# Kernel tuning notes

Measured on AMD Instinct MI355X. Metric: run time of the kernel, lower is better.

The kernel has to match this reference:

```python
import jax, jax.numpy as jnp
import numpy as np

N, G, E, H, M = 200000, 16, 400000, 400000, 800000
DN, DG, DE, DH, DM = 128, 32, 128, 64, 64
K_EDGE, K_HYP, AK = 32, 3, 8  # fixed incident edges per node, nodes per hyperedge, attention key size / heads
LN_EPS = 1e-3  # keras LayerNormalization default epsilon


def setup_inputs() -> dict:
    key = jax.random.key(0)
    ks = jax.random.split(key, 20)
    p = lambda k, shp: (0.02 * jax.random.normal(k, shp, dtype=jnp.float32))
    return {
        "nodes": jax.random.normal(ks[0], (N, DN), dtype=jnp.float32),
        "globals_": jax.random.normal(ks[1], (G, DG), dtype=jnp.float32),
        "n_node": jnp.full((G,), N // G, dtype=jnp.int32),
        "edges": jax.random.normal(ks[2], (E, DE), dtype=jnp.float32),
        "edge_ind": jax.random.randint(ks[3], (N, K_EDGE), 0, E, dtype=jnp.int32),
        "hfeat": jax.random.normal(ks[4], (H, DH), dtype=jnp.float32),
        "hind": jax.random.randint(ks[5], (H, K_HYP), 0, N, dtype=jnp.int32),
        "mfeat": jax.random.normal(ks[6], (M, DM), dtype=jnp.float32),
        "mind": jax.random.randint(ks[7], (M,), 0, N, dtype=jnp.int32),
        "Wq": p(ks[8], (DN, AK)), "bq": jnp.zeros((AK,), jnp.float32),
        "Wk": p(ks[9], (DE, AK)), "bk": jnp.zeros((AK,), jnp.float32),
        "Wc": p(ks[10], (4, AK, AK)), "bc": jnp.zeros((AK,), jnp.float32),
        "W1": p(ks[11], (DN + DG + AK + DH + DM, 256)), "b1": jnp.zeros((256,), jnp.float32),
        "W2": p(ks[12], (256, 128)), "b2": jnp.zeros((128,), jnp.float32),
        "ln_g": jnp.ones((128,), jnp.float32), "ln_b": jnp.zeros((128,), jnp.float32),
    }


def reference(nodes, globals_, n_node, edges, edge_ind, hfeat, hind, mfeat, mind,
              Wq, bq, Wk, bk, Wc, bc, W1, b1, W2, b2, ln_g, ln_b):
    n = nodes.shape[0]
    # _one_to_segments: repeat globals per node (graph id from n_node offsets)
    gid = jnp.searchsorted(jnp.cumsum(n_node), jnp.arange(n), side="right")
    g_per_node = globals_[gid]  # [N, DG]

    # EDGES branch: fixed-number multi-head attention over incident edges
    q = nodes @ Wq + bq   # [N, AK]
    k = edges @ Wk + bk   # [E, AK]
    # Conv1D(kernel=4, 'same') on a length-1 sequence: only kernel tap 1 touches data
    q_mh = q @ Wc[1] + bc  # [N, heads]
    k_mh = k @ Wc[1] + bc  # [E, heads]
    ek = k_mh[edge_ind]                         # [N, K, heads] gathered keys (= values)
    attn = jax.nn.softmax(q_mh[:, None, :] * ek, axis=1)
    edge_agg = jnp.sum(attn * ek, axis=1)       # [N, heads] (flatten of [N,1,heads])

    # _one_to_fixed_number: scatter hyperedge features to their K_HYP member nodes
    hh, kk, dh = hfeat.shape[0], hind.shape[1], hfeat.shape[1]
    h_agg = jax.ops.segment_sum(
        jnp.broadcast_to(hfeat[:, None, :], (hh, kk, dh)).reshape(hh * kk, dh),
        hind.reshape(-1), num_segments=n)       # [N, DH]

    # _one_to_unsorted_segments
    m_agg = jax.ops.segment_sum(mfeat, mind, num_segments=n)  # [N, DM]

    x = jnp.concatenate([nodes, g_per_node, edge_agg, h_agg, m_agg], axis=1)
    h1 = jax.nn.relu(x @ W1 + b1)
    h2 = jax.nn.relu(h1 @ W2 + b2)
    mu = jnp.mean(h2, axis=-1, keepdims=True)
    var = jnp.var(h2, axis=-1, keepdims=True)
    out = (h2 - mu) * jax.lax.rsqrt(var + LN_EPS) * ln_g + ln_b
    return out
```

## Files before the change

### kernel.cpp

```cpp
#include <hip/hip_runtime.h>
#include <hip/hip_bf16.h>
#include <math.h>

#define N_NODES 200000
#define N_E     400000
#define N_H     400000
#define N_M     800000
#define HK3     1200000
#define DIM_N   128
#define K_EDGE  32
#define D1      296
#define KX      320
#define LN_EPS  1e-3f
#define TILE    32
#define CHUNK   1024
#define NCH     196
#define NB_E    12500
#define NB_N    6250
#define NB_C    7813

typedef __attribute__((ext_vector_type(8))) short bf16x8;
typedef __attribute__((ext_vector_type(4))) float f32x4;
typedef unsigned short ushort_t;

#define SWZ(rr) (((rr) & 7) << 4)

__device__ __forceinline__ short f2bf(float f) {
    unsigned u = __float_as_uint(f);
    unsigned r = (u + 0x7fffu + ((u >> 16) & 1u)) >> 16;
    return (short)r;
}
__device__ __forceinline__ float bf2f(ushort_t u) {
    return __uint_as_float(((unsigned)u) << 16);
}
__device__ __forceinline__ void split2(float v, short& hi, short& lo) {
    hi = f2bf(v);
    float r = v - __uint_as_float(((unsigned)(ushort_t)hi) << 16);
    lo = f2bf(r);
}

__global__ void prep_weights(const float* __restrict__ Wq, const float* __restrict__ bq,
                             const float* __restrict__ Wk, const float* __restrict__ bk,
                             const float* __restrict__ Wc, const float* __restrict__ bc,
                             float* Wqc, float* bqc, float* Wkc, float* bkc) {
    int t = blockIdx.x * 256 + threadIdx.x;
    const float* Wc1 = Wc + 64;
    if (t < 128 * 8) {
        int i = t >> 3, o = t & 7;
        float s = 0.f, s2 = 0.f;
        for (int a = 0; a < 8; ++a) {
            float w = Wc1[a * 8 + o];
            s  += Wq[i * 8 + a] * w;
            s2 += Wk[i * 8 + a] * w;
        }
        Wqc[t] = s;
        Wkc[t] = s2;
    } else if (t < 128 * 8 + 8) {
        int o = t - 1024;
        float s = 0.f, s2 = 0.f;
        for (int a = 0; a < 8; ++a) {
            float w = Wc1[a * 8 + o];
            s  += bq[a] * w;
            s2 += bk[a] * w;
        }
        bqc[o] = s + bc[o];
        bkc[o] = s2 + bc[o];
    }
}

__global__ void prep_wF(const float* __restrict__ W1, const float* __restrict__ W2,
                        short* __restrict__ W1Fh, short* __restrict__ W1Fl,
                        short* __restrict__ W2Fh, short* __restrict__ W2Fl) {
    int g = blockIdx.x * 256 + threadIdx.x;
    if (g < 10240) {
        int l = g & 63, f = g >> 6;
        int s = f % 10, nt = (f / 10) & 3, wid = f / 40;
        int col = wid * 64 + nt * 16 + (l & 15);
        int k0 = s * 32 + (l >> 4) * 8;
        #pragma unroll
        for (int j = 0; j < 8; ++j) {
            int k = k0 + j;
            float w = (k < D1) ? W1[k * 256 + col] : 0.f;
            short hi, lo; split2(w, hi, lo);
            W1Fh[g * 8 + j] = hi; W1Fl[g * 8 + j] = lo;
        }
    } else if (g < 14336) {
        int u = g - 10240;
        int l = u & 63, f = u >> 6;
        int s = f & 7, nt = (f >> 3) & 1, wid = f >> 4;
        int col = wid * 32 + nt * 16 + (l & 15);
        int k0 = s * 32 + (l >> 4) * 8;
        #pragma unroll
        for (int j = 0; j < 8; ++j) {
            float w = W2[(k0 + j) * 128 + col];
            short hi, lo; split2(w, hi, lo);
            W2Fh[u * 8 + j] = hi; W2Fl[u * 8 + j] = lo;
        }
    }
}

__device__ __forceinline__ void mh_body(const float* __restrict__ feat,
                                        const float* __restrict__ Wf,
                                        const float* __restrict__ bf_,
                                        ushort_t* __restrict__ out8,
                                        int blk, int tid,
                                        float* el, float* wlT, float* bl) {
    for (int i = tid; i < 1024; i += 256) {
        int h = i >> 7, k = i & 127;
        wlT[h * 132 + k] = Wf[k * 8 + h];
    }
    if (tid < 8) bl[tid] = bf_[tid];
    long e0 = (long)blk * 32;
    const float4* ep = (const float4*)feat + e0 * 32;
    for (int it = 0; it < 4; ++it) {
        int idx = it * 256 + tid;
        int e = idx >> 5, f = idx & 31;
        float4 v = ep[e * 32 + f];
        float* d = &el[e * 132 + f * 4];
        d[0] = v.x; d[1] = v.y; d[2] = v.z; d[3] = v.w;
    }
    __syncthreads();
    int e = tid >> 3, h = tid & 7;
    float acc = bl[h];
    const float* er = &el[e * 132];
    const float* wr = &wlT[h * 132];
    #pragma unroll 8
    for (int i = 0; i < 128; i += 4) {
        float4 ev = *(const float4*)&er[i];
        float4 wv = *(const float4*)&wr[i];
        acc += ev.x * wv.x + ev.y * wv.y + ev.z * wv.z + ev.w * wv.w;
    }
    out8[(e0 + e) * 8 + h] = (ushort_t)f2bf(acc);
}

__global__ __launch_bounds__(256) void aux1_kernel(
    const float* __restrict__ edges, const float* __restrict__ Wkc,
    const float* __restrict__ bkc, ushort_t* __restrict__ kmh,
    const float* __restrict__ nodes, const float* __restrict__ Wqc,
    const float* __restrict__ bqc, ushort_t* __restrict__ qmh,
    const int* __restrict__ hind, const int* __restrict__ mind,
    int* __restrict__ cnth, int* __restrict__ cntm)
{
    __shared__ __align__(16) float el[32 * 132];
    __shared__ __align__(16) float wlT[8 * 132];
    __shared__ float bl[8];
    int b = blockIdx.x, tid = threadIdx.x;
    if (b < NB_E) {
        mh_body(edges, Wkc, bkc, kmh, b, tid, el, wlT, bl);
    } else if (b < NB_E + NB_N) {
        mh_body(nodes, Wqc, bqc, qmh, b - NB_E, tid, el, wlT, bl);
    } else {
        int t = (b - NB_E - NB_N) * 256 + tid;
        if (t < HK3)              atomicAdd(&cnth[hind[t]], 1);
        else if (t < HK3 + N_M)   atomicAdd(&cntm[mind[t - HK3]], 1);
    }
}

__global__ void zero_ints(int* __restrict__ p, int n) {
    int stride = gridDim.x * blockDim.x;
    for (int i = blockIdx.x * blockDim.x + threadIdx.x; i < n; i += stride) p[i] = 0;
}

__global__ __launch_bounds__(256) void sum_chunks(const int* __restrict__ cnth,
                                                  const int* __restrict__ cntm,
                                                  int* __restrict__ bsum) {
    int b = blockIdx.x;
    const int* cnt = (b < NCH) ? cnth : cntm;
    int base = ((b < NCH) ? b : b - NCH) * CHUNK;
    int tid = threadIdx.x;
    int s = 0;
    #pragma unroll
    for (int i = 0; i < 4; ++i) {
        int idx = base + i * 256 + tid;
        if (idx < N_NODES) s += cnt[idx];
    }
    __shared__ int sb[4];
    for (int d = 1; d < 64; d <<= 1) s += __shfl_xor(s, d);
    if ((tid & 63) == 0) sb[tid >> 6] = s;
    __syncthreads();
    if (tid == 0) bsum[b] = sb[0] + sb[1] + sb[2] + sb[3];
}

__global__ __launch_bounds__(256) void scan_sums(int* __restrict__ bsum) {
    __shared__ int sh[2][256];
    int tid = threadIdx.x;
    sh[0][tid] = (tid < NCH) ? bsum[tid] : 0;
    sh[1][tid] = (tid < NCH) ? bsum[NCH + tid] : 0;
    __syncthreads();
    for (int d = 1; d < 256; d <<= 1) {
        int v0 = (tid >= d) ? sh[0][tid - d] : 0;
        int v1 = (tid >= d) ? sh[1][tid - d] : 0;
        __syncthreads();
        sh[0][tid] += v0; sh[1][tid] += v1;
        __syncthreads();
    }
    if (tid < NCH) {
        bsum[tid]       = tid ? sh[0][tid - 1] : 0;
        bsum[NCH + tid] = tid ? sh[1][tid - 1] : 0;
    }
}

__global__ __launch_bounds__(256) void scan_chunks(const int* __restrict__ cnth,
                                                   const int* __restrict__ cntm,
                                                   const int* __restrict__ bsum,
                                                   int* __restrict__ offh, int* __restrict__ woffh,
                                                   int* __restrict__ offm, int* __restrict__ woffm) {
    int b = blockIdx.x;
    bool ish = (b < NCH);
    const int* cnt = ish ? cnth : cntm;
    int c = ish ? b : b - NCH;
    int* off  = ish ? offh  : offm;
    int* woff = ish ? woffh : woffm;
    int base = c * CHUNK;
    int tid = threadIdx.x;
    __shared__ int lds[CHUNK];
    __shared__ int tsum[256];
    #pragma unroll
    for (int i = 0; i < 4; ++i) {
        int idx = base + i * 256 + tid;
        lds[i * 256 + tid] = (idx < N_NODES) ? cnt[idx] : 0;
    }
    __syncthreads();
    int v0 = lds[tid * 4], v1 = lds[tid * 4 + 1], v2 = lds[tid * 4 + 2], v3 = lds[tid * 4 + 3];
    int tot = v0 + v1 + v2 + v3;
    tsum[tid] = tot;
    __syncthreads();
    for (int d = 1; d < 256; d <<= 1) {
        int v = (tid >= d) ? tsum[tid - d] : 0;
        __syncthreads();
        tsum[tid] += v;
        __syncthreads();
    }
    int pre = tsum[tid] - tot + bsum[b];
    int4 o;
    o.x = pre; o.y = pre + v0; o.z = pre + v0 + v1; o.w = pre + v0 + v1 + v2;
    int idx = base + tid * 4;
    if (idx + 3 < N_NODES) {
        *(int4*)(off + idx)  = o;
        *(int4*)(woff + idx) = o;
    } else {
        if (idx     < N_NODES) { off[idx]     = o.x; woff[idx]     = o.x; }
        if (idx + 1 < N_NODES) { off[idx + 1] = o.y; woff[idx + 1] = o.y; }
        if (idx + 2 < N_NODES) { off[idx + 2] = o.z; woff[idx + 2] = o.z; }
        if (idx + 3 < N_NODES) { off[idx + 3] = o.w; woff[idx + 3] = o.w; }
    }
}

__global__ void fill_kernel(const int* __restrict__ hind, const int* __restrict__ mind,
                            int* __restrict__ woffh, int* __restrict__ woffm,
                            int* __restrict__ listh, int* __restrict__ listm) {
    int t = blockIdx.x * 256 + threadIdx.x;
    if (t < HK3) {
        int node = hind[t];
        int pos = atomicAdd(&woffh[node], 1);
        listh[pos] = t / 3;
    } else if (t < HK3 + N_M) {
        int m = t - HK3;
        int node = mind[m];
        int pos = atomicAdd(&woffm[node], 1);
        listm[pos] = m;
    }
}

__global__ __launch_bounds__(256) void main_kernel(
    const float* __restrict__ nodes, const float* __restrict__ globals_,
    const int* __restrict__ n_node, const int* __restrict__ edge_ind,
    const ushort_t* __restrict__ kmh, const ushort_t* __restrict__ qmh,
    const float* __restrict__ hfeat, const int* __restrict__ offh,
    const int* __restrict__ woffh, const int* __restrict__ listh,
    const float* __restrict__ mfeat, const int* __restrict__ offm,
    const int* __restrict__ woffm, const int* __restrict__ listm,
    const short* __restrict__ W1Fh, const short* __restrict__ W1Fl, const float* __restrict__ b1,
    const short* __restrict__ W2Fh, const short* __restrict__ W2Fl, const float* __restrict__ b2,
    const float* __restrict__ ln_g, const float* __restrict__ ln_b,
    float* __restrict__ out)
{
    __shared__ __align__(16) char buf[20480];
    __shared__ int eind[32 * 33];
    __shared__ float mrs[64];

    int tid = threadIdx.x;
    int n0 = blockIdx.x * TILE;
    char* xhi = buf;

    const float4* np4 = (const float4*)nodes;
    #pragma unroll
    for (int it = 0; it < 4; ++it) {
        int idx = it * 256 + tid;
        int r = idx >> 5, c4 = idx & 31;
        float4 v = np4[(size_t)(n0 + r) * 32 + c4];
        short4 hi;
        hi.x = f2bf(v.x); hi.y = f2bf(v.y); hi.z = f2bf(v.z); hi.w = f2bf(v.w);
        *(short4*)(xhi + r * 640 + ((c4 * 8) ^ SWZ(r))) = hi;
    }
    {
        int nn0 = n_node[0];
        int r = tid >> 3, c4 = tid & 7;
        int gid = (n0 + r) / nn0;
        float4 v = ((const float4*)globals_)[gid * 8 + c4];
        short4 hi;
        hi.x = f2bf(v.x); hi.y = f2bf(v.y); hi.z = f2bf(v.z); hi.w = f2bf(v.w);
        *(short4*)(xhi + r * 640 + ((256 + c4 * 8) ^ SWZ(r))) = hi;
    }
    {
        int r = tid >> 3, q = tid & 7;
        int n = n0 + r;
        float a[8];
        #pragma unroll
        for (int i = 0; i < 8; ++i) a[i] = 0.f;
        int e0 = offh[n], e1 = woffh[n];
        int e = e0;
        #define ACC8(U, V) do { \
            a[0] += (U).x; a[1] += (U).y; a[2] += (U).z; a[3] += (U).w; \
            a[4] += (V).x; a[5] += (V).y; a[6] += (V).z; a[7] += (V).w; } while (0)
        for (; e + 4 <= e1; e += 4) {
            int i0 = listh[e], i1 = listh[e + 1], i2 = listh[e + 2], i3 = listh[e + 3];
            const float4* p0 = (const float4*)(hfeat + (size_t)i0 * 64 + q * 8);
            const float4* p1 = (const float4*)(hfeat + (size_t)i1 * 64 + q * 8);
            const float4* p2 = (const float4*)(hfeat + (size_t)i2 * 64 + q * 8);
            const float4* p3 = (const float4*)(hfeat + (size_t)i3 * 64 + q * 8);
            float4 u0 = p0[0], v0 = p0[1];
            float4 u1 = p1[0], v1 = p1[1];
            float4 u2 = p2[0], v2 = p2[1];
            float4 u3 = p3[0], v3 = p3[1];
            ACC8(u0, v0); ACC8(u1, v1); ACC8(u2, v2); ACC8(u3, v3);
        }
        for (; e < e1; ++e) {
            const float4* p = (const float4*)(hfeat + (size_t)listh[e] * 64 + q * 8);
            float4 u = p[0], v = p[1];
            ACC8(u, v);
        }
        {
            bf16x8 hi;
            #pragma unroll
            for (int i = 0; i < 8; ++i) hi[i] = f2bf(a[i]);
            *(bf16x8*)(xhi + r * 640 + ((336 + q * 16) ^ SWZ(r))) = hi;
        }
        #pragma unroll
        for (int i = 0; i < 8; ++i) a[i] = 0.f;
        e0 = offm[n]; e1 = woffm[n];
        e = e0;
        for (; e + 4 <= e1; e += 4) {
            int i0 = listm[e], i1 = listm[e + 1], i2 = listm[e + 2], i3 = listm[e + 3];
            const float4* p0 = (const float4*)(mfeat + (size_t)i0 * 64 + q * 8);
            const float4* p1 = (const float4*)(mfeat + (size_t)i1 * 64 + q * 8);
            const float4* p2 = (const float4*)(mfeat + (size_t)i2 * 64 + q * 8);
            const float4* p3 = (const float4*)(mfeat + (size_t)i3 * 64 + q * 8);
            float4 u0 = p0[0], v0 = p0[1];
            float4 u1 = p1[0], v1 = p1[1];
            float4 u2 = p2[0], v2 = p2[1];
            float4 u3 = p3[0], v3 = p3[1];
            ACC8(u0, v0); ACC8(u1, v1); ACC8(u2, v2); ACC8(u3, v3);
        }
        for (; e < e1; ++e) {
            const float4* p = (const float4*)(mfeat + (size_t)listm[e] * 64 + q * 8);
            float4 u = p[0], v = p[1];
            ACC8(u, v);
        }
        #undef ACC8
        {
            bf16x8 hi;
            #pragma unroll
            for (int i = 0; i < 8; ++i) hi[i] = f2bf(a[i]);
            *(bf16x8*)(xhi + r * 640 + ((464 + q * 16) ^ SWZ(r))) = hi;
        }
    }
    if (tid < 192) {
        short4 z = { 0, 0, 0, 0 };
        int r = tid / 6, j = tid % 6;
        *(short4*)(xhi + r * 640 + ((592 + j * 8) ^ SWZ(r))) = z;
    }
    #pragma unroll
    for (int it = 0; it < 4; ++it) {
        int idx = it * 256 + tid;
        int r = idx >> 5, j = idx & 31;
        eind[r * 33 + j] = edge_ind[(size_t)(n0 + r) * 32 + j];
    }
    __syncthreads();

    {
        int r = tid & 31, h = tid >> 5;
        float qv = bf2f(qmh[(size_t)(n0 + r) * 8 + h]);
        float m = -INFINITY, s = 0.f, wv = 0.f;
        for (int j = 0; j < K_EDGE; ++j) {
            int e = eind[r * 33 + j];
            float v = bf2f(kmh[(size_t)e * 8 + h]);
            float l = qv * v;
            float mn = fmaxf(m, l);
            float fac = __expf(m - mn);
            float p = __expf(l - mn);
            s = s * fac + p;
            wv = wv * fac + p * v;
            m = mn;
        }
        *(short*)(xhi + r * 640 + ((320 + h * 2) ^ SWZ(r))) = f2bf(wv / s);
    }
    __syncthreads();

    int wid = tid >> 6, lane = tid & 63;
    int arow = lane & 15, kgrp = lane >> 4;
    f32x4 c1[2][4];
    #pragma unroll
    for (int mt = 0; mt < 2; ++mt)
        #pragma unroll
        for (int nt = 0; nt < 4; ++nt)
            c1[mt][nt] = (f32x4){0.f, 0.f, 0.f, 0.f};
    const bf16x8* w1h = (const bf16x8*)W1Fh;
    const bf16x8* w1l = (const bf16x8*)W1Fl;
    for (int s = 0; s < 10; ++s) {
        int kb = (s * 32 + kgrp * 8) * 2;
        bf16x8 ahv[2], bh[4], bl[4];
        #pragma unroll
        for (int mt = 0; mt < 2; ++mt) {
            int rr = mt * 16 + arow;
            ahv[mt] = *(const bf16x8*)(xhi + rr * 640 + (kb ^ SWZ(rr)));
        }
        #pragma unroll
        for (int nt = 0; nt < 4; ++nt) {
            size_t fi = ((size_t)(wid * 4 + nt) * 10 + s) * 64 + lane;
            bh[nt] = w1h[fi];
            bl[nt] = w1l[fi];
        }
        #pragma unroll
        for (int mt = 0; mt < 2; ++mt)
            #pragma unroll
            for (int nt = 0; nt < 4; ++nt) {
                c1[mt][nt] = __builtin_amdgcn_mfma_f32_16x16x32_bf16(ahv[mt], bh[nt], c1[mt][nt], 0, 0, 0);
                c1[mt][nt] = __builtin_amdgcn_mfma_f32_16x16x32_bf16(ahv[mt], bl[nt], c1[mt][nt], 0, 0, 0);
            }
    }
    __syncthreads();
    char* h1p = buf;
    #pragma unroll
    for (int nt = 0; nt < 4; ++nt) {
        int col = wid * 64 + nt * 16 + arow;
        float bb = b1[col];
        #pragma unroll
        for (int mt = 0; mt < 2; ++mt)
            #pragma unroll
            for (int i = 0; i < 4; ++i) {
                int rr = mt * 16 + kgrp * 4 + i;
                float v = fmaxf(c1[mt][nt][i] + bb, 0.f);
                *(short*)(h1p + rr * 512 + ((col * 2) ^ SWZ(rr))) = f2bf(v);
            }
    }
    __syncthreads();

    f32x4 c2[2][2];
    #pragma unroll
    for (int mt = 0; mt < 2; ++mt)
        #pragma unroll
        for (int nt = 0; nt < 2; ++nt)
            c2[mt][nt] = (f32x4){0.f, 0.f, 0.f, 0.f};
    const bf16x8* w2h = (const bf16x8*)W2Fh;
    const bf16x8* w2l = (const bf16x8*)W2Fl;
    for (int s = 0; s < 8; ++s) {
        int kb = (s * 32 + kgrp * 8) * 2;
        bf16x8 ahv[2], bh[2], bl[2];
        #pragma unroll
        for (int mt = 0; mt < 2; ++mt) {
            int rr = mt * 16 + arow;
            ahv[mt] = *(const bf16x8*)(h1p + rr * 512 + (kb ^ SWZ(rr)));
        }
        #pragma unroll
        for (int nt = 0; nt < 2; ++nt) {
            size_t fi = ((size_t)(wid * 2 + nt) * 8 + s) * 64 + lane;
            bh[nt] = w2h[fi];
            bl[nt] = w2l[fi];
        }
        #pragma unroll
        for (int mt = 0; mt < 2; ++mt)
            #pragma unroll
            for (int nt = 0; nt < 2; ++nt) {
                c2[mt][nt] = __builtin_amdgcn_mfma_f32_16x16x32_bf16(ahv[mt], bh[nt], c2[mt][nt], 0, 0, 0);
                c2[mt][nt] = __builtin_amdgcn_mfma_f32_16x16x32_bf16(ahv[mt], bl[nt], c2[mt][nt], 0, 0, 0);
            }
    }
    __syncthreads();
    #pragma unroll
    for (int nt = 0; nt < 2; ++nt) {
        int col = wid * 32 + nt * 16 + arow;
        float bb = b2[col];
        #pragma unroll
        for (int mt = 0; mt < 2; ++mt)
            #pragma unroll
            for (int i = 0; i < 4; ++i) {
                int rr = mt * 16 + kgrp * 4 + i;
                *(float*)(buf + rr * 528 + col * 4) = fmaxf(c2[mt][nt][i] + bb, 0.f);
            }
    }
    __syncthreads();

    {
        int r = tid >> 3, q = tid & 7;
        const float* row = (const float*)(buf + r * 528) + q * 16;
        float s = 0.f, sq = 0.f;
        #pragma unroll
        for (int j = 0; j < 4; ++j) {
            float4 v = *(const float4*)(row + j * 4);
            s  += v.x + v.y + v.z + v.w;
            sq += v.x * v.x + v.y * v.y + v.z * v.z + v.w * v.w;
        }
        s  += __shfl_xor(s, 1);  sq += __shfl_xor(sq, 1);
        s  += __shfl_xor(s, 2);  sq += __shfl_xor(sq, 2);
        s  += __shfl_xor(s, 4);  sq += __shfl_xor(sq, 4);
        if (q == 0) {
            float mean = s * (1.f / 128.f);
            float var = sq * (1.f / 128.f) - mean * mean;
            mrs[r] = mean;
            mrs[32 + r] = rsqrtf(var + LN_EPS);
        }
    }
    __syncthreads();
    #pragma unroll
    for (int it = 0; it < 4; ++it) {
        int idx = it * 256 + tid;
        int r = idx >> 5, c4 = idx & 31;
        float4 v = *(const float4*)(buf + r * 528 + c4 * 16);
        float mu = mrs[r], rs = mrs[32 + r];
        float4 g = ((const float4*)ln_g)[c4];
        float4 bb = ((const float4*)ln_b)[c4];
        float4 o;
        o.x = (v.x - mu) * rs * g.x + bb.x;
        o.y = (v.y - mu) * rs * g.y + bb.y;
        o.z = (v.z - mu) * rs * g.z + bb.z;
        o.w = (v.w - mu) * rs * g.w + bb.w;
        ((float4*)out)[(size_t)(n0 + r) * 32 + c4] = o;
    }
}

extern "C" void kernel_launch(void* const* d_in, const int* in_sizes, int n_in,
                              void* d_out, int out_size, void* d_ws, size_t ws_size,
                              hipStream_t stream) {
    const float* nodes    = (const float*)d_in[0];
    const float* globals_ = (const float*)d_in[1];
    const int*   n_node   = (const int*)  d_in[2];
    const float* edges    = (const float*)d_in[3];
    const int*   edge_ind = (const int*)  d_in[4];
    const float* hfeat    = (const float*)d_in[5];
    const int*   hind     = (const int*)  d_in[6];
    const float* mfeat    = (const float*)d_in[7];
    const int*   mind     = (const int*)  d_in[8];
    const float* Wq       = (const float*)d_in[9];
    const float* bq       = (const float*)d_in[10];
    const float* Wk       = (const float*)d_in[11];
    const float* bk       = (const float*)d_in[12];
    const float* Wc       = (const float*)d_in[13];
    const float* bc       = (const float*)d_in[14];
    const float* W1       = (const float*)d_in[15];
    const float* b1       = (const float*)d_in[16];
    const float* W2       = (const float*)d_in[17];
    const float* b2       = (const float*)d_in[18];
    const float* ln_g     = (const float*)d_in[19];
    const float* ln_b     = (const float*)d_in[20];
    float* out = (float*)d_out;

    char* w = (char*)d_ws;
    size_t off = 0;
    auto take = [&](size_t bytes) -> char* {
        char* p = w + off;
        off = (off + bytes + 255) & ~(size_t)255;
        return p;
    };
    float*    Wqc  = (float*)take(1024 * 4);
    float*    bqc  = (float*)take(8 * 4);
    float*    Wkc  = (float*)take(1024 * 4);
    float*    bkc  = (float*)take(8 * 4);
    short*    W1Fh = (short*)take(256 * KX * 2);
    short*    W1Fl = (short*)take(256 * KX * 2);
    short*    W2Fh = (short*)take(128 * 256 * 2);
    short*    W2Fl = (short*)take(128 * 256 * 2);
    ushort_t* kmh  = (ushort_t*)take((size_t)N_E * 8 * 2);
    ushort_t* qmh  = (ushort_t*)take((size_t)N_NODES * 8 * 2);
    int*      cnth = (int*)take((size_t)N_NODES * 4);
    int*      cntm = (int*)take((size_t)N_NODES * 4);
    int*      offh = (int*)take((size_t)N_NODES * 4);
    int*      woffh= (int*)take((size_t)N_NODES * 4);
    int*      offm = (int*)take((size_t)N_NODES * 4);
    int*      woffm= (int*)take((size_t)N_NODES * 4);
    int*      listh= (int*)take((size_t)HK3 * 4);
    int*      listm= (int*)take((size_t)N_M * 4);
    int*      bsum = (int*)take(2 * NCH * 4);
    (void)ws_size;

    prep_weights<<<5, 256, 0, stream>>>(Wq, bq, Wk, bk, Wc, bc, Wqc, bqc, Wkc, bkc);
    prep_wF<<<56, 256, 0, stream>>>(W1, W2, W1Fh, W1Fl, W2Fh, W2Fl);
    zero_ints<<<512, 256, 0, stream>>>(cnth, 2 * N_NODES);
    aux1_kernel<<<NB_E + NB_N + NB_C, 256, 0, stream>>>(
        edges, Wkc, bkc, kmh, nodes, Wqc, bqc, qmh, hind, mind, cnth, cntm);
    sum_chunks<<<2 * NCH, 256, 0, stream>>>(cnth, cntm, bsum);
    scan_sums<<<1, 256, 0, stream>>>(bsum);
    scan_chunks<<<2 * NCH, 256, 0, stream>>>(cnth, cntm, bsum, offh, woffh, offm, woffm);
    fill_kernel<<<(HK3 + N_M + 255) / 256, 256, 0, stream>>>(hind, mind, woffh, woffm, listh, listm);
    main_kernel<<<N_NODES / TILE, 256, 0, stream>>>(
        nodes, globals_, n_node, edge_ind, kmh, qmh,
        hfeat, offh, woffh, listh, mfeat, offm, woffm, listm,
        W1Fh, W1Fl, b1, W2Fh, W2Fl, b2, ln_g, ln_b, out);
}
```

Measured before the change: 691.1 us.

## Vectorize CSR fill, interleave hyper/message gathers, raise MFMA wave priority

The fill kernel now handles four indices per thread using int4 loads, cutting the thread count by four while keeping the atomics. In the main kernel, the hyperedge and message gather loops are interleaved so both streams issue loads together, which exposes more memory-level parallelism. s_setprio is raised around the MFMA loops to favour matrix-issuing waves. The interleaving adds register pressure that could reduce occupancy.

```diff
diff --git a/kernel.cpp b/kernel.cpp
--- a/kernel.cpp
+++ b/kernel.cpp
@@ -246,19 +246,26 @@
     }
 }
 
-__global__ void fill_kernel(const int* __restrict__ hind, const int* __restrict__ mind,
-                            int* __restrict__ woffh, int* __restrict__ woffm,
-                            int* __restrict__ listh, int* __restrict__ listm) {
+__global__ __launch_bounds__(256) void fill_kernel(
+    const int* __restrict__ hind, const int* __restrict__ mind,
+    int* __restrict__ woffh, int* __restrict__ woffm,
+    int* __restrict__ listh, int* __restrict__ listm) {
     int t = blockIdx.x * 256 + threadIdx.x;
-    if (t < HK3) {
-        int node = hind[t];
-        int pos = atomicAdd(&woffh[node], 1);
-        listh[pos] = t / 3;
-    } else if (t < HK3 + N_M) {
-        int m = t - HK3;
-        int node = mind[m];
-        int pos = atomicAdd(&woffm[node], 1);
-        listm[pos] = m;
+    if (t < HK3 / 4) {
+        int4 nd = ((const int4*)hind)[t];
+        int base = t * 4;
+        int p0 = atomicAdd(&woffh[nd.x], 1); listh[p0] = (base    ) / 3;
+        int p1 = atomicAdd(&woffh[nd.y], 1); listh[p1] = (base + 1) / 3;
+        int p2 = atomicAdd(&woffh[nd.z], 1); listh[p2] = (base + 2) / 3;
+        int p3 = atomicAdd(&woffh[nd.w], 1); listh[p3] = (base + 3) / 3;
+    } else if (t < HK3 / 4 + N_M / 4) {
+        int u = t - HK3 / 4;
+        int4 nd = ((const int4*)mind)[u];
+        int base = u * 4;
+        int p0 = atomicAdd(&woffm[nd.x], 1); listm[p0] = base;
+        int p1 = atomicAdd(&woffm[nd.y], 1); listm[p1] = base + 1;
+        int p2 = atomicAdd(&woffm[nd.z], 1); listm[p2] = base + 2;
+        int p3 = atomicAdd(&woffm[nd.w], 1); listm[p3] = base + 3;
     }
 }
 
@@ -305,63 +312,70 @@
     {
         int r = tid >> 3, q = tid & 7;
         int n = n0 + r;
-        float a[8];
-        #pragma unroll
-        for (int i = 0; i < 8; ++i) a[i] = 0.f;
-        int e0 = offh[n], e1 = woffh[n];
-        int e = e0;
-        #define ACC8(U, V) do { \
-            a[0] += (U).x; a[1] += (U).y; a[2] += (U).z; a[3] += (U).w; \
-            a[4] += (V).x; a[5] += (V).y; a[6] += (V).z; a[7] += (V).w; } while (0)
-        for (; e + 4 <= e1; e += 4) {
-            int i0 = listh[e], i1 = listh[e + 1], i2 = listh[e + 2], i3 = listh[e + 3];
-            const float4* p0 = (const float4*)(hfeat + (size_t)i0 * 64 + q * 8);
-            const float4* p1 = (const float4*)(hfeat + (size_t)i1 * 64 + q * 8);
-            const float4* p2 = (const float4*)(hfeat + (size_t)i2 * 64 + q * 8);
-            const float4* p3 = (const float4*)(hfeat + (size_t)i3 * 64 + q * 8);
-            float4 u0 = p0[0], v0 = p0[1];
-            float4 u1 = p1[0], v1 = p1[1];
-            float4 u2 = p2[0], v2 = p2[1];
-            float4 u3 = p3[0], v3 = p3[1];
-            ACC8(u0, v0); ACC8(u1, v1); ACC8(u2, v2); ACC8(u3, v3);
-        }
-        for (; e < e1; ++e) {
-            const float4* p = (const float4*)(hfeat + (size_t)listh[e] * 64 + q * 8);
+        float ah[8], am[8];
+        #pragma unroll
+        for (int i = 0; i < 8; ++i) { ah[i] = 0.f; am[i] = 0.f; }
+        int eh = offh[n], ehe = woffh[n];
+        int em = offm[n], eme = woffm[n];
+        #define ACC8(A, U, V) do { \
+            A[0] += (U).x; A[1] += (U).y; A[2] += (U).z; A[3] += (U).w; \
+            A[4] += (V).x; A[5] += (V).y; A[6] += (V).z; A[7] += (V).w; } while (0)
+        for (; eh + 4 <= ehe && em + 4 <= eme; eh += 4, em += 4) {
+            int h0 = listh[eh], h1_ = listh[eh + 1], h2_ = listh[eh + 2], h3 = listh[eh + 3];
+            int m0 = listm[em], m1 = listm[em + 1], m2 = listm[em + 2], m3 = listm[em + 3];
+            const float4* ph0 = (const float4*)(hfeat + (size_t)h0  * 64 + q * 8);
+            const float4* ph1 = (const float4*)(hfeat + (size_t)h1_ * 64 + q * 8);
+            const float4* ph2 = (const float4*)(hfeat + (size_t)h2_ * 64 + q * 8);
+            const float4* ph3 = (const float4*)(hfeat + (size_t)h3  * 64 + q * 8);
+            const float4* pm0 = (const float4*)(mfeat + (size_t)m0 * 64 + q * 8);
+            const float4* pm1 = (const float4*)(mfeat + (size_t)m1 * 64 + q * 8);
+            const float4* pm2 = (const float4*)(mfeat + (size_t)m2 * 64 + q * 8);
+            const float4* pm3 = (const float4*)(mfeat + (size_t)m3 * 64 + q * 8);
+            float4 hu0 = ph0[0], hv0 = ph0[1], hu1 = ph1[0], hv1 = ph1[1];
+            float4 hu2 = ph2[0], hv2 = ph2[1], hu3 = ph3[0], hv3 = ph3[1];
+            float4 mu0 = pm0[0], mv0 = pm0[1], mu1 = pm1[0], mv1 = pm1[1];
+            float4 mu2 = pm2[0], mv2 = pm2[1], mu3 = pm3[0], mv3 = pm3[1];
+            ACC8(ah, hu0, hv0); ACC8(ah, hu1, hv1); ACC8(ah, hu2, hv2); ACC8(ah, hu3, hv3);
+            ACC8(am, mu0, mv0); ACC8(am, mu1, mv1); ACC8(am, mu2, mv2); ACC8(am, mu3, mv3);
+        }
+        for (; eh + 4 <= ehe; eh += 4) {
+            int h0 = listh[eh], h1_ = listh[eh + 1], h2_ = listh[eh + 2], h3 = listh[eh + 3];
+            const float4* p0 = (const float4*)(hfeat + (size_t)h0  * 64 + q * 8);
+            const float4* p1 = (const float4*)(hfeat + (size_t)h1_ * 64 + q * 8);
+            const float4* p2 = (const float4*)(hfeat + (size_t)h2_ * 64 + q * 8);
+            const float4* p3 = (const float4*)(hfeat + (size_t)h3  * 64 + q * 8);
+            float4 u0 = p0[0], v0 = p0[1], u1 = p1[0], v1 = p1[1];
+            float4 u2 = p2[0], v2 = p2[1], u3 = p3[0], v3 = p3[1];
+            ACC8(ah, u0, v0); ACC8(ah, u1, v1); ACC8(ah, u2, v2); ACC8(ah, u3, v3);
+        }
+        for (; eh < ehe; ++eh) {
+            const float4* p = (const float4*)(hfeat + (size_t)listh[eh] * 64 + q * 8);
             float4 u = p[0], v = p[1];
-            ACC8(u, v);
-        }
-        {
-            bf16x8 hi;
-            #pragma unroll
-            for (int i = 0; i < 8; ++i) hi[i] = f2bf(a[i]);
-            *(bf16x8*)(xhi + r * 640 + ((336 + q * 16) ^ SWZ(r))) = hi;
-        }
-        #pragma unroll
-        for (int i = 0; i < 8; ++i) a[i] = 0.f;
-        e0 = offm[n]; e1 = woffm[n];
-        e = e0;
-        for (; e + 4 <= e1; e += 4) {
-            int i0 = listm[e], i1 = listm[e + 1], i2 = listm[e + 2], i3 = listm[e + 3];
-            const float4* p0 = (const float4*)(mfeat + (size_t)i0 * 64 + q * 8);
-            const float4* p1 = (const float4*)(mfeat + (size_t)i1 * 64 + q * 8);
-            const float4* p2 = (const float4*)(mfeat + (size_t)i2 * 64 + q * 8);
-            const float4* p3 = (const float4*)(mfeat + (size_t)i3 * 64 + q * 8);
-            float4 u0 = p0[0], v0 = p0[1];
-            float4 u1 = p1[0], v1 = p1[1];
-            float4 u2 = p2[0], v2 = p2[1];
-            float4 u3 = p3[0], v3 = p3[1];
-            ACC8(u0, v0); ACC8(u1, v1); ACC8(u2, v2); ACC8(u3, v3);
-        }
-        for (; e < e1; ++e) {
-            const float4* p = (const float4*)(mfeat + (size_t)listm[e] * 64 + q * 8);
+            ACC8(ah, u, v);
+        }
+        for (; em + 4 <= eme; em += 4) {
+            int m0 = listm[em], m1 = listm[em + 1], m2 = listm[em + 2], m3 = listm[em + 3];
+            const float4* p0 = (const float4*)(mfeat + (size_t)m0 * 64 + q * 8);
+            const float4* p1 = (const float4*)(mfeat + (size_t)m1 * 64 + q * 8);
+            const float4* p2 = (const float4*)(mfeat + (size_t)m2 * 64 + q * 8);
+            const float4* p3 = (const float4*)(mfeat + (size_t)m3 * 64 + q * 8);
+            float4 u0 = p0[0], v0 = p0[1], u1 = p1[0], v1 = p1[1];
+            float4 u2 = p2[0], v2 = p2[1], u3 = p3[0], v3 = p3[1];
+            ACC8(am, u0, v0); ACC8(am, u1, v1); ACC8(am, u2, v2); ACC8(am, u3, v3);
+        }
+        for (; em < eme; ++em) {
+            const float4* p = (const float4*)(mfeat + (size_t)listm[em] * 64 + q * 8);
             float4 u = p[0], v = p[1];
-            ACC8(u, v);
+            ACC8(am, u, v);
         }
         #undef ACC8
         {
             bf16x8 hi;
             #pragma unroll
-            for (int i = 0; i < 8; ++i) hi[i] = f2bf(a[i]);
+            for (int i = 0; i < 8; ++i) hi[i] = f2bf(ah[i]);
+            *(bf16x8*)(xhi + r * 640 + ((336 + q * 16) ^ SWZ(r))) = hi;
+            #pragma unroll
+            for (int i = 0; i < 8; ++i) hi[i] = f2bf(am[i]);
             *(bf16x8*)(xhi + r * 640 + ((464 + q * 16) ^ SWZ(r))) = hi;
         }
     }
@@ -407,6 +421,7 @@
             c1[mt][nt] = (f32x4){0.f, 0.f, 0.f, 0.f};
     const bf16x8* w1h = (const bf16x8*)W1Fh;
     const bf16x8* w1l = (const bf16x8*)W1Fl;
+    __builtin_amdgcn_s_setprio(1);
     for (int s = 0; s < 10; ++s) {
         int kb = (s * 32 + kgrp * 8) * 2;
         bf16x8 ahv[2], bh[4], bl[4];
@@ -429,6 +444,7 @@
                 c1[mt][nt] = __builtin_amdgcn_mfma_f32_16x16x32_bf16(ahv[mt], bl[nt], c1[mt][nt], 0, 0, 0);
             }
     }
+    __builtin_amdgcn_s_setprio(0);
     __syncthreads();
     char* h1p = buf;
     #pragma unroll
@@ -454,6 +470,7 @@
             c2[mt][nt] = (f32x4){0.f, 0.f, 0.f, 0.f};
     const bf16x8* w2h = (const bf16x8*)W2Fh;
     const bf16x8* w2l = (const bf16x8*)W2Fl;
+    __builtin_amdgcn_s_setprio(1);
     for (int s = 0; s < 8; ++s) {
         int kb = (s * 32 + kgrp * 8) * 2;
         bf16x8 ahv[2], bh[2], bl[2];
@@ -476,6 +493,7 @@
                 c2[mt][nt] = __builtin_amdgcn_mfma_f32_16x16x32_bf16(ahv[mt], bl[nt], c2[mt][nt], 0, 0, 0);
             }
     }
+    __builtin_amdgcn_s_setprio(0);
     __syncthreads();
     #pragma unroll
     for (int nt = 0; nt < 2; ++nt) {
@@ -591,7 +609,8 @@
     sum_chunks<<<2 * NCH, 256, 0, stream>>>(cnth, cntm, bsum);
     scan_sums<<<1, 256, 0, stream>>>(bsum);
     scan_chunks<<<2 * NCH, 256, 0, stream>>>(cnth, cntm, bsum, offh, woffh, offm, woffm);
-    fill_kernel<<<(HK3 + N_M + 255) / 256, 256, 0, stream>>>(hind, mind, woffh, woffm, listh, listm);
+    fill_kernel<<<(HK3 / 4 + N_M / 4 + 255) / 256, 256, 0, stream>>>(
+        hind, mind, woffh, woffm, listh, listm);
     main_kernel<<<N_NODES / TILE, 256, 0, stream>>>(
         nodes, globals_, n_node, edge_ind, kmh, qmh,
         hfeat, offh, woffh, listh, mfeat, offm, woffm, listm,
```

After: 737.9 us. +6.8%, slower.
